# Optimization experiments

Measured on AMD Instinct MI355X. Metric: run time of the kernel, lower is better.

The kernel has to match this reference:

```python
import jax, jax.numpy as jnp
import numpy as np

N_NODES = 50000
N_EDGES = 1600000
IN_CH = 32
HID = 64
K = 2


def _dconv(X, edge_index, edge_weight, W, b):
    """Diffusion graph conv (torch_geometric_temporal DConv, K=2).

    X: [N, C_in], W: [2, K, C_in, C_out], b: [C_out].
    Direction 0: forward transition P_f = D_out^{-1} A  (applied as P_f^T X).
    Direction 1: backward transition P_b = D_in^{-1} A^T (applied as P_b^T X).
    """
    n = X.shape[0]
    row, col = edge_index[0], edge_index[1]
    deg_out = jax.ops.segment_sum(edge_weight, row, num_segments=n)  # out-degree (row sums of A)
    deg_in = jax.ops.segment_sum(edge_weight, col, num_segments=n)   # in-degree  (col sums of A)
    norm_out = edge_weight / deg_out[row]  # [E]
    norm_in = edge_weight / deg_in[col]    # [E]

    # k = 0 term: identity for both directions
    H = X @ (W[0, 0] + W[1, 0])

    # k = 1 term: one diffusion step in each direction
    # forward dir: out[i] = sum_{(j->i)} w/deg_out[j] * X[j]
    Tx_o = jax.ops.segment_sum(norm_out[:, None] * X[row], col, num_segments=n)
    # backward dir: out[i] = sum_{(i->j)} w/deg_in[j] * X[j]
    Tx_i = jax.ops.segment_sum(norm_in[:, None] * X[col], row, num_segments=n)
    H = H + Tx_o @ W[0, 1] + Tx_i @ W[1, 1]
    return H + b


def setup_inputs() -> dict:
    key = jax.random.key(0)
    ks = jax.random.split(key, 12)
    cat_ch = IN_CH + HID  # GRU concatenates [X, H]
    s = 1.0 / np.sqrt(cat_ch)
    inp = {
        "x": jax.random.normal(ks[0], (N_NODES, IN_CH), dtype=jnp.float32),
        "edge_index": jax.random.randint(ks[1], (2, N_EDGES), 0, N_NODES, dtype=jnp.int32),
        "edge_weight": jax.random.uniform(ks[2], (N_EDGES,), dtype=jnp.float32, minval=0.05, maxval=1.0),
        "Wz": jax.random.uniform(ks[3], (2, K, cat_ch, HID), dtype=jnp.float32, minval=-s, maxval=s),
        "bz": jnp.zeros((HID,), dtype=jnp.float32),
        "Wr": jax.random.uniform(ks[4], (2, K, cat_ch, HID), dtype=jnp.float32, minval=-s, maxval=s),
        "br": jnp.zeros((HID,), dtype=jnp.float32),
        "Wh": jax.random.uniform(ks[5], (2, K, cat_ch, HID), dtype=jnp.float32, minval=-s, maxval=s),
        "bh": jnp.zeros((HID,), dtype=jnp.float32),
        "Wlin": jax.random.uniform(ks[6], (HID, 1), dtype=jnp.float32, minval=-1.0 / np.sqrt(HID), maxval=1.0 / np.sqrt(HID)),
        "blin": jnp.zeros((1,), dtype=jnp.float32),
    }
    return inp


def reference(x, edge_index, edge_weight, Wz, bz, Wr, br, Wh, bh, Wlin, blin):
    n = x.shape[0]
    H0 = jnp.zeros((n, HID), dtype=x.dtype)  # initial hidden state (H=None)
    XH = jnp.concatenate([x, H0], axis=-1)   # [N, IN_CH+HID]
    Z = jax.nn.sigmoid(_dconv(XH, edge_index, edge_weight, Wz, bz))
    R = jax.nn.sigmoid(_dconv(XH, edge_index, edge_weight, Wr, br))
    XHR = jnp.concatenate([x, H0 * R], axis=-1)
    H_tilde = jnp.tanh(_dconv(XHR, edge_index, edge_weight, Wh, bh))
    H = Z * H0 + (1.0 - Z) * H_tilde
    out = jnp.maximum(H, 0.0) @ Wlin + blin  # ReLU then Linear(hidden, 1)
    return out
```

## Files before the change

### kernel.cpp

```cpp
#include <hip/hip_runtime.h>
#include <math.h>

#define N_NODES 50000
#define N_EDGES 1600000
#define IN_CH 32
#define HID 64

#define NBIN 391
#define BIN_SHIFT 7
#define CHUNK 4096
#define NCHK ((N_EDGES + CHUNK - 1) / CHUNK)
#define CNTG_N (2 * NBIN * NCHK)
#define CNTG_N4 ((CNTG_N + 3) / 4)
#define SCAN_BLOCKS ((CNTG_N4 + 1023) / 1024)
#define FG_CAP 4608

#define WS_RDEG_OUT 0
#define WS_RDEG_IN  50000
#define WS_CNTG     100000
#define WS_BLKSUM   405764
#define WS_WBF      405892
#define WS_BINCNT   412036
#define WS_XSB      512132
#define WS_TXO      1312132
#define WS_TXI      2112132
#define WS_BINNED   2912132
#define WS_END      9312132

typedef __attribute__((ext_vector_type(8))) short bf16x8;
typedef __attribute__((ext_vector_type(4))) float f32x4;

__device__ __forceinline__ unsigned short f2bf(float f) {
    unsigned int u = __float_as_uint(f);
    return (unsigned short)((u + 0x7fffu + ((u >> 16) & 1u)) >> 16);
}
__device__ __forceinline__ float bf2f(unsigned short b) {
    return __uint_as_float((unsigned int)b << 16);
}

__global__ __launch_bounds__(256) void wprep_kernel(
    const float* __restrict__ Wz, const float* __restrict__ Wh,
    unsigned short* __restrict__ wbf) {
    int idx = blockIdx.x * 256 + threadIdx.x;
    if (idx >= 12288) return;
    int j = idx & 7, ln = (idx >> 3) & 63, bn = (idx >> 9) & 7, kk = idx >> 12;
    int k = kk * 32 + (ln >> 4) * 8 + j;
    int n = bn * 16 + (ln & 15);
    int slab = k >> 5, c = k & 31;
    const float* W = (n < 64) ? Wz : Wh;
    int o = n & 63;
    float v;
    if (slab == 0)      v = W[c * 64 + o] + W[(2 * 96 + c) * 64 + o];
    else if (slab == 1) v = W[(96 + c) * 64 + o];
    else                v = W[(3 * 96 + c) * 64 + o];
    wbf[idx] = f2bf(v);
}

__global__ __launch_bounds__(256) void xconv_kernel(
    const float4* __restrict__ x4, ushort4* __restrict__ xsb) {
    int i = blockIdx.x * 256 + threadIdx.x;
    if (i >= N_NODES * 8) return;
    float4 v = x4[i];
    ushort4 o;
    o.x = f2bf(v.x); o.y = f2bf(v.y); o.z = f2bf(v.z); o.w = f2bf(v.w);
    xsb[i] = o;
}

__global__ __launch_bounds__(512) void hist_kernel(const int* __restrict__ ei,
                                                   int* __restrict__ cntG) {
    __shared__ int h[2 * NBIN];
    int tid = threadIdx.x;
    for (int i = tid; i < 2 * NBIN; i += 512) h[i] = 0;
    __syncthreads();
    int e0 = blockIdx.x * CHUNK;
    int e1 = min(e0 + CHUNK, N_EDGES);
    for (int e = e0 + tid; e < e1; e += 512) {
        int r = ei[e];
        int c = ei[N_EDGES + e];
        atomicAdd(&h[c >> BIN_SHIFT], 1);
        atomicAdd(&h[NBIN + (r >> BIN_SHIFT)], 1);
    }
    __syncthreads();
    for (int i = tid; i < 2 * NBIN; i += 512) cntG[i * NCHK + blockIdx.x] = h[i];
}

__global__ __launch_bounds__(256) void scan_partial_kernel(
    const int4* __restrict__ cnt4, int* __restrict__ blksum, int n4) {
    __shared__ int s[256];
    int t = threadIdx.x;
    int base4 = blockIdx.x * 1024 + t * 4;
    int total = 0;
#pragma unroll
    for (int j = 0; j < 4; ++j) {
        int idx = base4 + j;
        if (idx < n4) {
            int4 v = cnt4[idx];
            total += v.x + v.y + v.z + v.w;
        }
    }
    s[t] = total;
    __syncthreads();
    for (int off = 128; off > 0; off >>= 1) {
        if (t < off) s[t] += s[t + off];
        __syncthreads();
    }
    if (t == 0) blksum[blockIdx.x] = s[0];
}

__global__ __launch_bounds__(256) void scan_blocksum_kernel(int* __restrict__ blksum, int nb) {
    __shared__ int s[256];
    int t = threadIdx.x;
    int v = (t < nb) ? blksum[t] : 0;
    s[t] = v;
    __syncthreads();
    for (int off = 1; off < 256; off <<= 1) {
        int u = (t >= off) ? s[t - off] : 0;
        __syncthreads();
        s[t] += u;
        __syncthreads();
    }
    if (t < nb) blksum[t] = s[t] - v;
}

__global__ __launch_bounds__(256) void scan_final_kernel(
    int4* __restrict__ cnt4, const int* __restrict__ blksum, int n4) {
    __shared__ int s[256];
    int t = threadIdx.x;
    int base4 = blockIdx.x * 1024 + t * 4;
    int4 vals[4];
    int total = 0;
#pragma unroll
    for (int j = 0; j < 4; ++j) {
        int idx = base4 + j;
        vals[j] = (idx < n4) ? cnt4[idx] : make_int4(0, 0, 0, 0);
        total += vals[j].x + vals[j].y + vals[j].z + vals[j].w;
    }
    s[t] = total;
    __syncthreads();
    for (int off = 1; off < 256; off <<= 1) {
        int u = (t >= off) ? s[t - off] : 0;
        __syncthreads();
        s[t] += u;
        __syncthreads();
    }
    int run = blksum[blockIdx.x] + s[t] - total;
#pragma unroll
    for (int j = 0; j < 4; ++j) {
        int idx = base4 + j;
        int4 v = vals[j];
        int4 o;
        o.x = run; run += v.x;
        o.y = run; run += v.y;
        o.z = run; run += v.z;
        o.w = run; run += v.w;
        if (idx < n4) cnt4[idx] = o;
    }
}

__global__ __launch_bounds__(512) void partition_kernel(
    const int* __restrict__ ei, const float* __restrict__ ew,
    const int* __restrict__ cntG, int2* __restrict__ binned) {
    __shared__ int2 stg[CHUNK];
    __shared__ int hist[NBIN];
    __shared__ int gStart[NBIN];
    __shared__ int sc[512];
    int tid = threadIdx.x;
    int dir = (blockIdx.x >= NCHK) ? 1 : 0;
    int chunk = blockIdx.x - dir * NCHK;

    for (int i = tid; i < NBIN; i += 512) hist[i] = 0;
    __syncthreads();

    int e0 = chunk * CHUNK;
    int n_e = min(CHUNK, N_EDGES - e0);
    int binv[8], rankv[8];
    int2 pay[8];
#pragma unroll
    for (int j = 0; j < 8; ++j) {
        int idx = tid + j * 512;
        if (idx < n_e) {
            int e = e0 + idx;
            int r = ei[e];
            int c = ei[N_EDGES + e];
            int dst = dir ? r : c;
            int src = dir ? c : r;
            int b = dst >> BIN_SHIFT;
            binv[j] = b;
            rankv[j] = atomicAdd(&hist[b], 1);
            pay[j] = make_int2((int)(((unsigned)b << 23) | ((unsigned)(dst & 127) << 16) |
                                     (unsigned)src),
                               __float_as_int(ew[e]));
        } else {
            binv[j] = -1;
        }
    }
    __syncthreads();
    int v = (tid < NBIN) ? hist[tid] : 0;
    sc[tid] = v;
    __syncthreads();
    for (int off = 1; off < 512; off <<= 1) {
        int u = (tid >= off) ? sc[tid - off] : 0;
        __syncthreads();
        sc[tid] += u;
        __syncthreads();
    }
    if (tid < NBIN) {
        hist[tid] = sc[tid] - v;
        gStart[tid] = cntG[(dir * NBIN + tid) * NCHK + chunk];
    }
    __syncthreads();
#pragma unroll
    for (int j = 0; j < 8; ++j)
        if (binv[j] >= 0) stg[hist[binv[j]] + rankv[j]] = pay[j];
    __syncthreads();
    for (int p = tid; p < n_e; p += 512) {
        int2 v2 = stg[p];
        int b = (int)(((unsigned)v2.x) >> 23);
        int gpos = gStart[b] + (p - hist[b]);
        binned[gpos] = make_int2(v2.x & 0x7FFFFF, v2.y);
    }
}

__device__ __forceinline__ void bin_range(const int* cntG, int b, int& lo, int& hi) {
    lo = cntG[b * NCHK];
    hi = (b + 1 < 2 * NBIN) ? cntG[(b + 1) * NCHK] : 2 * N_EDGES;
}

__global__ __launch_bounds__(512) void bindeg_kernel(
    const int* __restrict__ cntG, const int2* __restrict__ binned,
    int* __restrict__ binCnt, float* __restrict__ ws_f) {
    __shared__ float wsum[128];
    __shared__ int cnt[128];
    int tid = threadIdx.x;
    int b = blockIdx.x;
    int dir = (b >= NBIN) ? 1 : 0;
    if (tid < 128) { wsum[tid] = 0.f; cnt[tid] = 0; }
    __syncthreads();
    int lo, hi;
    bin_range(cntG, b, lo, hi);
    for (int p = lo + tid; p < hi; p += 512) {
        int2 v = binned[p];
        int d = v.x >> 16;
        atomicAdd(&cnt[d], 1);
        atomicAdd(&wsum[d], __int_as_float(v.y));
    }
    __syncthreads();
    if (tid < 128) {
        binCnt[b * 128 + tid] = cnt[tid];
        int node = (b - dir * NBIN) * 128 + tid;
        if (node < N_NODES) {
            float s = wsum[tid];
            float* rdeg = ws_f + (dir == 0 ? WS_RDEG_IN : WS_RDEG_OUT);
            rdeg[node] = (s != 0.f) ? (1.f / s) : 0.f;
        }
    }
}

__global__ __launch_bounds__(512) void fgather_kernel(
    const ushort4* __restrict__ xsb, const int* __restrict__ cntG,
    const int* __restrict__ binCnt, const int2* __restrict__ binned,
    float* __restrict__ ws_f) {
    __shared__ int2 s_edge[FG_CAP];
    __shared__ int s_off[129];
    __shared__ int s_cur[128];
    __shared__ int sc[128];
    int tid = threadIdx.x;
    int b = blockIdx.x;
    int dir = (b >= NBIN) ? 1 : 0;
    int bin = b - dir * NBIN;

    int v = (tid < 128) ? binCnt[b * 128 + tid] : 0;
    if (tid < 128) sc[tid] = v;
    __syncthreads();
    for (int off = 1; off < 128; off <<= 1) {
        int u = (tid < 128 && tid >= off) ? sc[tid - off] : 0;
        __syncthreads();
        if (tid < 128) sc[tid] += u;
        __syncthreads();
    }
    if (tid < 128) {
        s_off[tid] = sc[tid] - v;
        s_cur[tid] = sc[tid] - v;
    }
    if (tid == 127) s_off[128] = sc[127];
    __syncthreads();

    int lo, hi;
    bin_range(cntG, b, lo, hi);
    int n_e = hi - lo;
    for (int p = tid; p < n_e; p += 512) {
        int2 ev = binned[lo + p];
        int rk = atomicAdd(&s_cur[ev.x >> 16], 1);
        if (rk < FG_CAP) s_edge[rk] = ev;
    }
    __syncthreads();

    const float* rdeg = ws_f + (dir == 0 ? WS_RDEG_OUT : WS_RDEG_IN);
    ushort4* outp = (ushort4*)(ws_f + (dir == 0 ? WS_TXO : WS_TXI));
    int lane = tid & 7;
#pragma unroll
    for (int it = 0; it < 2; ++it) {
        int nl = it * 64 + (tid >> 3);
        int p = s_off[nl], end = s_off[nl + 1];
        float4 acc = make_float4(0.f, 0.f, 0.f, 0.f);
        for (; p + 1 < end; p += 2) {
            int2 v0 = s_edge[p], v1 = s_edge[p + 1];
            int s0 = v0.x & 0xffff, s1 = v1.x & 0xffff;
            float c0 = __int_as_float(v0.y) * rdeg[s0];
            float c1 = __int_as_float(v1.y) * rdeg[s1];
            ushort4 a = xsb[s0 * 8 + lane];
            ushort4 bb = xsb[s1 * 8 + lane];
            acc.x += c0 * bf2f(a.x) + c1 * bf2f(bb.x);
            acc.y += c0 * bf2f(a.y) + c1 * bf2f(bb.y);
            acc.z += c0 * bf2f(a.z) + c1 * bf2f(bb.z);
            acc.w += c0 * bf2f(a.w) + c1 * bf2f(bb.w);
        }
        if (p < end) {
            int2 v0 = s_edge[p];
            int s0 = v0.x & 0xffff;
            float c0 = __int_as_float(v0.y) * rdeg[s0];
            ushort4 a = xsb[s0 * 8 + lane];
            acc.x += c0 * bf2f(a.x);
            acc.y += c0 * bf2f(a.y);
            acc.z += c0 * bf2f(a.z);
            acc.w += c0 * bf2f(a.w);
        }
        int node = bin * 128 + nl;
        if (node < N_NODES) {
            ushort4 o;
            o.x = f2bf(acc.x); o.y = f2bf(acc.y);
            o.z = f2bf(acc.z); o.w = f2bf(acc.w);
            outp[node * 8 + lane] = o;
        }
    }
}

#define DN_GROUP 64
#define DN_BLOCKS ((N_NODES + DN_GROUP - 1) / DN_GROUP)
__global__ __launch_bounds__(256) void dense_kernel(
    const float4* __restrict__ x4,
    const int4* __restrict__ txo_b, const int4* __restrict__ txi_b,
    const unsigned short* __restrict__ wbf,
    const float* __restrict__ bz, const float* __restrict__ bh,
    const float* __restrict__ Wlin, const float* __restrict__ blin,
    float* __restrict__ out) {
    __shared__ unsigned short sA[64 * 104];
    __shared__ unsigned short sB[12288];

    int tid = threadIdx.x;
    int lane = tid & 63, w = tid >> 6;
    int lm = lane & 15, quad = lane >> 4;

    for (int idx = tid; idx < 3072; idx += 256)
        *(ushort4*)&sB[idx * 4] = ((const ushort4*)wbf)[idx];

    int node0 = blockIdx.x * DN_GROUP;
    for (int idx = tid; idx < 64 * 8; idx += 256) {
        int nl = idx >> 3, q = idx & 7;
        int node = node0 + nl;
        float4 v = (node < N_NODES) ? x4[node * 8 + q]
                                    : make_float4(0.f, 0.f, 0.f, 0.f);
        ushort4 bq;
        bq.x = f2bf(v.x); bq.y = f2bf(v.y); bq.z = f2bf(v.z); bq.w = f2bf(v.w);
        *(ushort4*)&sA[nl * 104 + q * 4] = bq;
    }
    for (int idx = tid; idx < 64 * 8; idx += 256) {
        int nl = idx >> 3, q = idx & 7;
        int node = node0 + nl;
        int4 v = make_int4(0, 0, 0, 0);
        if (node < N_NODES)
            v = (q < 4) ? txo_b[node * 4 + q] : txi_b[node * 4 + (q - 4)];
        *(int4*)&sA[nl * 104 + 32 + q * 8] = v;
    }

    float bzv[4], bhv[4], wlv[4];
#pragma unroll
    for (int bn = 0; bn < 4; ++bn) {
        int o = lm + 16 * bn;
        bzv[bn] = bz[o]; bhv[bn] = bh[o]; wlv[bn] = Wlin[o];
    }
    float bl = blin[0];
    __syncthreads();

    f32x4 acc[8];
#pragma unroll
    for (int bn = 0; bn < 4; ++bn) {
        acc[bn]     = (f32x4){bzv[bn], bzv[bn], bzv[bn], bzv[bn]};
        acc[bn + 4] = (f32x4){bhv[bn], bhv[bn], bhv[bn], bhv[bn]};
    }
#pragma unroll
    for (int kk = 0; kk < 3; ++kk) {
        bf16x8 af = *(const bf16x8*)&sA[(w * 16 + lm) * 104 + kk * 32 + quad * 8];
#pragma unroll
        for (int bn = 0; bn < 8; ++bn) {
            bf16x8 bf = *(const bf16x8*)&sB[((kk * 8 + bn) * 64 + lane) * 8];
            acc[bn] = __builtin_amdgcn_mfma_f32_16x16x32_bf16(af, bf, acc[bn], 0, 0, 0);
        }
    }

    float partial[4] = {0.f, 0.f, 0.f, 0.f};
#pragma unroll
    for (int bn = 0; bn < 4; ++bn) {
#pragma unroll
        for (int reg = 0; reg < 4; ++reg) {
            float az = acc[bn][reg], ah = acc[bn + 4][reg];
            float z = 1.f / (1.f + __expf(-az));
            float ht = 1.f - 2.f / (__expf(2.f * ah) + 1.f);
            partial[reg] += fmaxf((1.f - z) * ht, 0.f) * wlv[bn];
        }
    }
#pragma unroll
    for (int reg = 0; reg < 4; ++reg) {
        float s = partial[reg];
        s += __shfl_xor(s, 1, 64);
        s += __shfl_xor(s, 2, 64);
        s += __shfl_xor(s, 4, 64);
        s += __shfl_xor(s, 8, 64);
        if (lm == 0) {
            int node = node0 + w * 16 + quad * 4 + reg;
            if (node < N_NODES) out[node] = s + bl;
        }
    }
}

extern "C" void kernel_launch(void* const* d_in, const int* in_sizes, int n_in,
                              void* d_out, int out_size, void* d_ws, size_t ws_size,
                              hipStream_t stream) {
    const float* x = (const float*)d_in[0];
    const int* ei = (const int*)d_in[1];
    const float* ew = (const float*)d_in[2];
    const float* Wz = (const float*)d_in[3];
    const float* bz = (const float*)d_in[4];
    const float* Wh = (const float*)d_in[7];
    const float* bh = (const float*)d_in[8];
    const float* Wlin = (const float*)d_in[9];
    const float* blin = (const float*)d_in[10];
    float* out = (float*)d_out;
    float* wf = (float*)d_ws;
    int* wi = (int*)d_ws;
    int2* binned = (int2*)(wi + WS_BINNED);

    wprep_kernel<<<48, 256, 0, stream>>>(Wz, Wh, (unsigned short*)(wi + WS_WBF));
    xconv_kernel<<<(N_NODES * 8 + 255) / 256, 256, 0, stream>>>(
        (const float4*)x, (ushort4*)(wi + WS_XSB));
    hist_kernel<<<NCHK, 512, 0, stream>>>(ei, wi + WS_CNTG);
    scan_partial_kernel<<<SCAN_BLOCKS, 256, 0, stream>>>(
        (const int4*)(wi + WS_CNTG), wi + WS_BLKSUM, CNTG_N4);
    scan_blocksum_kernel<<<1, 256, 0, stream>>>(wi + WS_BLKSUM, SCAN_BLOCKS);
    scan_final_kernel<<<SCAN_BLOCKS, 256, 0, stream>>>(
        (int4*)(wi + WS_CNTG), wi + WS_BLKSUM, CNTG_N4);
    partition_kernel<<<2 * NCHK, 512, 0, stream>>>(ei, ew, wi + WS_CNTG, binned);
    bindeg_kernel<<<2 * NBIN, 512, 0, stream>>>(
        wi + WS_CNTG, binned, wi + WS_BINCNT, wf);
    fgather_kernel<<<2 * NBIN, 512, 0, stream>>>(
        (const ushort4*)(wi + WS_XSB), wi + WS_CNTG, wi + WS_BINCNT, binned, wf);
    dense_kernel<<<DN_BLOCKS, 256, 0, stream>>>(
        (const float4*)x, (const int4*)(wi + WS_TXO), (const int4*)(wi + WS_TXI),
        (const unsigned short*)(wi + WS_WBF), bz, bh, Wlin, blin, out);
}
```

Measured before the change: 198.1 us.

## Halve destination bins, double partition chunk, precompute edge coefficients in gather

Bins shrink from 128 to 64 destination nodes, which doubles the bin count and halves block size in the degree and gather kernels. Partition chunks double to 8192 edges, with a paired-bin scan so 512 threads still cover the histogram. The gather kernel now multiplies edge weight by reciprocal degree during staging rather than in the inner loop, and unrolls the inner loop by four to expose more independent loads. The aim is more parallelism and fewer dependent loads in the gather, at the cost of more bins, more scan entries and a smaller per-bin shared-memory capacity that could overflow on skewed graphs.

```diff
diff --git a/kernel.cpp b/kernel.cpp
--- a/kernel.cpp
+++ b/kernel.cpp
@@ -6,26 +6,26 @@
 #define IN_CH 32
 #define HID 64
 
-#define NBIN 391
-#define BIN_SHIFT 7
-#define CHUNK 4096
+#define NBIN 782
+#define BIN_SHIFT 6
+#define CHUNK 8192
 #define NCHK ((N_EDGES + CHUNK - 1) / CHUNK)
 #define CNTG_N (2 * NBIN * NCHK)
-#define CNTG_N4 ((CNTG_N + 3) / 4)
+#define CNTG_N4 (CNTG_N / 4)
 #define SCAN_BLOCKS ((CNTG_N4 + 1023) / 1024)
-#define FG_CAP 4608
+#define FG_CAP 2560
 
 #define WS_RDEG_OUT 0
 #define WS_RDEG_IN  50000
 #define WS_CNTG     100000
-#define WS_BLKSUM   405764
-#define WS_WBF      405892
-#define WS_BINCNT   412036
-#define WS_XSB      512132
-#define WS_TXO      1312132
-#define WS_TXI      2112132
-#define WS_BINNED   2912132
-#define WS_END      9312132
+#define WS_BLKSUM   406548
+#define WS_WBF      406676
+#define WS_BINCNT   412820
+#define WS_XSB      512916
+#define WS_TXO      1312916
+#define WS_TXI      2112916
+#define WS_BINNED   2912916
+#define WS_END      9312916
 
 typedef __attribute__((ext_vector_type(8))) short bf16x8;
 typedef __attribute__((ext_vector_type(4))) float f32x4;
@@ -162,6 +162,7 @@
     const int* __restrict__ cntG, int2* __restrict__ binned) {
     __shared__ int2 stg[CHUNK];
     __shared__ int hist[NBIN];
+    __shared__ int lst[NBIN];
     __shared__ int gStart[NBIN];
     __shared__ int sc[512];
     int tid = threadIdx.x;
@@ -173,10 +174,10 @@
 
     int e0 = chunk * CHUNK;
     int n_e = min(CHUNK, N_EDGES - e0);
-    int binv[8], rankv[8];
-    int2 pay[8];
-#pragma unroll
-    for (int j = 0; j < 8; ++j) {
+    int binv[16], rankv[16];
+    int2 pay[16];
+#pragma unroll
+    for (int j = 0; j < 16; ++j) {
         int idx = tid + j * 512;
         if (idx < n_e) {
             int e = e0 + idx;
@@ -187,7 +188,7 @@
             int b = dst >> BIN_SHIFT;
             binv[j] = b;
             rankv[j] = atomicAdd(&hist[b], 1);
-            pay[j] = make_int2((int)(((unsigned)b << 23) | ((unsigned)(dst & 127) << 16) |
+            pay[j] = make_int2((int)(((unsigned)b << 22) | ((unsigned)(dst & 63) << 16) |
                                      (unsigned)src),
                                __float_as_int(ew[e]));
         } else {
@@ -195,8 +196,8 @@
         }
     }
     __syncthreads();
-    int v = (tid < NBIN) ? hist[tid] : 0;
-    sc[tid] = v;
+    int ps = (tid < 391) ? (hist[2 * tid] + hist[2 * tid + 1]) : 0;
+    sc[tid] = ps;
     __syncthreads();
     for (int off = 1; off < 512; off <<= 1) {
         int u = (tid >= off) ? sc[tid - off] : 0;
@@ -204,20 +205,23 @@
         sc[tid] += u;
         __syncthreads();
     }
-    if (tid < NBIN) {
-        hist[tid] = sc[tid] - v;
-        gStart[tid] = cntG[(dir * NBIN + tid) * NCHK + chunk];
-    }
-    __syncthreads();
-#pragma unroll
-    for (int j = 0; j < 8; ++j)
-        if (binv[j] >= 0) stg[hist[binv[j]] + rankv[j]] = pay[j];
+    if (tid < 391) {
+        int pref = sc[tid] - ps;
+        lst[2 * tid] = pref;
+        lst[2 * tid + 1] = pref + hist[2 * tid];
+    }
+    for (int i = tid; i < NBIN; i += 512)
+        gStart[i] = cntG[(dir * NBIN + i) * NCHK + chunk];
+    __syncthreads();
+#pragma unroll
+    for (int j = 0; j < 16; ++j)
+        if (binv[j] >= 0) stg[lst[binv[j]] + rankv[j]] = pay[j];
     __syncthreads();
     for (int p = tid; p < n_e; p += 512) {
         int2 v2 = stg[p];
-        int b = (int)(((unsigned)v2.x) >> 23);
-        int gpos = gStart[b] + (p - hist[b]);
-        binned[gpos] = make_int2(v2.x & 0x7FFFFF, v2.y);
+        int b = (int)(((unsigned)v2.x) >> 22);
+        int gpos = gStart[b] + (p - lst[b]);
+        binned[gpos] = make_int2(v2.x & 0x3FFFFF, v2.y);
     }
 }
 
@@ -226,28 +230,28 @@
     hi = (b + 1 < 2 * NBIN) ? cntG[(b + 1) * NCHK] : 2 * N_EDGES;
 }
 
-__global__ __launch_bounds__(512) void bindeg_kernel(
+__global__ __launch_bounds__(256) void bindeg_kernel(
     const int* __restrict__ cntG, const int2* __restrict__ binned,
     int* __restrict__ binCnt, float* __restrict__ ws_f) {
-    __shared__ float wsum[128];
-    __shared__ int cnt[128];
+    __shared__ float wsum[64];
+    __shared__ int cnt[64];
     int tid = threadIdx.x;
     int b = blockIdx.x;
     int dir = (b >= NBIN) ? 1 : 0;
-    if (tid < 128) { wsum[tid] = 0.f; cnt[tid] = 0; }
+    if (tid < 64) { wsum[tid] = 0.f; cnt[tid] = 0; }
     __syncthreads();
     int lo, hi;
     bin_range(cntG, b, lo, hi);
-    for (int p = lo + tid; p < hi; p += 512) {
+    for (int p = lo + tid; p < hi; p += 256) {
         int2 v = binned[p];
         int d = v.x >> 16;
         atomicAdd(&cnt[d], 1);
         atomicAdd(&wsum[d], __int_as_float(v.y));
     }
     __syncthreads();
-    if (tid < 128) {
-        binCnt[b * 128 + tid] = cnt[tid];
-        int node = (b - dir * NBIN) * 128 + tid;
+    if (tid < 64) {
+        binCnt[b * 64 + tid] = cnt[tid];
+        int node = (b - dir * NBIN) * 64 + tid;
         if (node < N_NODES) {
             float s = wsum[tid];
             float* rdeg = ws_f + (dir == 0 ? WS_RDEG_IN : WS_RDEG_OUT);
@@ -256,76 +260,79 @@
     }
 }
 
-__global__ __launch_bounds__(512) void fgather_kernel(
+__global__ __launch_bounds__(256) void fgather_kernel(
     const ushort4* __restrict__ xsb, const int* __restrict__ cntG,
     const int* __restrict__ binCnt, const int2* __restrict__ binned,
     float* __restrict__ ws_f) {
     __shared__ int2 s_edge[FG_CAP];
-    __shared__ int s_off[129];
-    __shared__ int s_cur[128];
-    __shared__ int sc[128];
+    __shared__ int s_off[65];
+    __shared__ int s_cur[64];
+    __shared__ int sc[64];
     int tid = threadIdx.x;
     int b = blockIdx.x;
     int dir = (b >= NBIN) ? 1 : 0;
     int bin = b - dir * NBIN;
 
-    int v = (tid < 128) ? binCnt[b * 128 + tid] : 0;
-    if (tid < 128) sc[tid] = v;
-    __syncthreads();
-    for (int off = 1; off < 128; off <<= 1) {
-        int u = (tid < 128 && tid >= off) ? sc[tid - off] : 0;
-        __syncthreads();
-        if (tid < 128) sc[tid] += u;
-        __syncthreads();
-    }
-    if (tid < 128) {
+    int v = (tid < 64) ? binCnt[b * 64 + tid] : 0;
+    if (tid < 64) sc[tid] = v;
+    __syncthreads();
+    for (int off = 1; off < 64; off <<= 1) {
+        int u = (tid < 64 && tid >= off) ? sc[tid - off] : 0;
+        __syncthreads();
+        if (tid < 64) sc[tid] += u;
+        __syncthreads();
+    }
+    if (tid < 64) {
         s_off[tid] = sc[tid] - v;
         s_cur[tid] = sc[tid] - v;
     }
-    if (tid == 127) s_off[128] = sc[127];
-    __syncthreads();
-
+    if (tid == 63) s_off[64] = sc[63];
+    __syncthreads();
+
+    const float* rdeg = ws_f + (dir == 0 ? WS_RDEG_OUT : WS_RDEG_IN);
     int lo, hi;
     bin_range(cntG, b, lo, hi);
     int n_e = hi - lo;
-    for (int p = tid; p < n_e; p += 512) {
+    for (int p = tid; p < n_e; p += 256) {
         int2 ev = binned[lo + p];
+        int src = ev.x & 0xffff;
+        float coef = __int_as_float(ev.y) * rdeg[src];
         int rk = atomicAdd(&s_cur[ev.x >> 16], 1);
-        if (rk < FG_CAP) s_edge[rk] = ev;
-    }
-    __syncthreads();
-
-    const float* rdeg = ws_f + (dir == 0 ? WS_RDEG_OUT : WS_RDEG_IN);
+        if (rk < FG_CAP) s_edge[rk] = make_int2(src, __float_as_int(coef));
+    }
+    __syncthreads();
+
     ushort4* outp = (ushort4*)(ws_f + (dir == 0 ? WS_TXO : WS_TXI));
     int lane = tid & 7;
 #pragma unroll
     for (int it = 0; it < 2; ++it) {
-        int nl = it * 64 + (tid >> 3);
+        int nl = it * 32 + (tid >> 3);
         int p = s_off[nl], end = s_off[nl + 1];
         float4 acc = make_float4(0.f, 0.f, 0.f, 0.f);
-        for (; p + 1 < end; p += 2) {
+        for (; p + 3 < end; p += 4) {
             int2 v0 = s_edge[p], v1 = s_edge[p + 1];
-            int s0 = v0.x & 0xffff, s1 = v1.x & 0xffff;
-            float c0 = __int_as_float(v0.y) * rdeg[s0];
-            float c1 = __int_as_float(v1.y) * rdeg[s1];
-            ushort4 a = xsb[s0 * 8 + lane];
-            ushort4 bb = xsb[s1 * 8 + lane];
-            acc.x += c0 * bf2f(a.x) + c1 * bf2f(bb.x);
-            acc.y += c0 * bf2f(a.y) + c1 * bf2f(bb.y);
-            acc.z += c0 * bf2f(a.z) + c1 * bf2f(bb.z);
-            acc.w += c0 * bf2f(a.w) + c1 * bf2f(bb.w);
-        }
-        if (p < end) {
+            int2 v2 = s_edge[p + 2], v3 = s_edge[p + 3];
+            ushort4 a0 = xsb[v0.x * 8 + lane];
+            ushort4 a1 = xsb[v1.x * 8 + lane];
+            ushort4 a2 = xsb[v2.x * 8 + lane];
+            ushort4 a3 = xsb[v3.x * 8 + lane];
+            float c0 = __int_as_float(v0.y), c1 = __int_as_float(v1.y);
+            float c2 = __int_as_float(v2.y), c3 = __int_as_float(v3.y);
+            acc.x += c0 * bf2f(a0.x) + c1 * bf2f(a1.x) + c2 * bf2f(a2.x) + c3 * bf2f(a3.x);
+            acc.y += c0 * bf2f(a0.y) + c1 * bf2f(a1.y) + c2 * bf2f(a2.y) + c3 * bf2f(a3.y);
+            acc.z += c0 * bf2f(a0.z) + c1 * bf2f(a1.z) + c2 * bf2f(a2.z) + c3 * bf2f(a3.z);
+            acc.w += c0 * bf2f(a0.w) + c1 * bf2f(a1.w) + c2 * bf2f(a2.w) + c3 * bf2f(a3.w);
+        }
+        for (; p < end; ++p) {
             int2 v0 = s_edge[p];
-            int s0 = v0.x & 0xffff;
-            float c0 = __int_as_float(v0.y) * rdeg[s0];
-            ushort4 a = xsb[s0 * 8 + lane];
+            float c0 = __int_as_float(v0.y);
+            ushort4 a = xsb[v0.x * 8 + lane];
             acc.x += c0 * bf2f(a.x);
             acc.y += c0 * bf2f(a.y);
             acc.z += c0 * bf2f(a.z);
             acc.w += c0 * bf2f(a.w);
         }
-        int node = bin * 128 + nl;
+        int node = bin * 64 + nl;
         if (node < N_NODES) {
             ushort4 o;
             o.x = f2bf(acc.x); o.y = f2bf(acc.y);
@@ -450,9 +457,9 @@
     scan_final_kernel<<<SCAN_BLOCKS, 256, 0, stream>>>(
         (int4*)(wi + WS_CNTG), wi + WS_BLKSUM, CNTG_N4);
     partition_kernel<<<2 * NCHK, 512, 0, stream>>>(ei, ew, wi + WS_CNTG, binned);
-    bindeg_kernel<<<2 * NBIN, 512, 0, stream>>>(
+    bindeg_kernel<<<2 * NBIN, 256, 0, stream>>>(
         wi + WS_CNTG, binned, wi + WS_BINCNT, wf);
-    fgather_kernel<<<2 * NBIN, 512, 0, stream>>>(
+    fgather_kernel<<<2 * NBIN, 256, 0, stream>>>(
         (const ushort4*)(wi + WS_XSB), wi + WS_CNTG, wi + WS_BINCNT, binned, wf);
     dense_kernel<<<DN_BLOCKS, 256, 0, stream>>>(
         (const float4*)x, (const int4*)(wi + WS_TXO), (const int4*)(wi + WS_TXI),
```

Result: no change. 196.1 us (-1.0%).
